# Optimization experiments

Hardware: AMD Instinct MI355X
Metric: run time of the kernel (lower is better)

Reference implementation:

```python
import jax, jax.numpy as jnp
import numpy as np

B, C, H, W = 8, 256, 64, 64
CR = C // 8  # reduced channels for query/key


def setup_inputs() -> dict:
    key = jax.random.key(0)
    ks = jax.random.split(key, 10)
    s = 0.02
    return {
        "x": jax.random.normal(ks[0], (B, C, H, W), dtype=jnp.float32),
        "cross_modal_features": jax.random.normal(ks[1], (B, C, H, W), dtype=jnp.float32),
        "wq": jax.random.normal(ks[2], (CR, C), dtype=jnp.float32) * s,
        "bq": jnp.zeros((CR,), dtype=jnp.float32),
        "wk": jax.random.normal(ks[3], (CR, C), dtype=jnp.float32) * s,
        "bk": jnp.zeros((CR,), dtype=jnp.float32),
        "wv": jax.random.normal(ks[4], (C, C), dtype=jnp.float32) * s,
        "bv": jnp.zeros((C,), dtype=jnp.float32),
        "wo": jax.random.normal(ks[5], (C, C), dtype=jnp.float32) * s,
        "bo": jnp.zeros((C,), dtype=jnp.float32),
        "gamma": jnp.zeros((1,), dtype=jnp.float32),
    }


def _conv1x1(w, b, t):
    # t: (B, Cin, HW) -> (B, Cout, HW); 1x1 conv == channel matmul
    return jnp.einsum("oc,bcn->bon", w, t) + b[None, :, None]


def reference(x, cross_modal_features, wq, bq, wk, bk, wv, bv, wo, bo, gamma):
    b, c, h, w = x.shape
    n = h * w
    xf = x.reshape(b, c, n)
    ff = cross_modal_features.reshape(b, c, n)
    q = _conv1x1(wq, bq, xf)          # (B, CR, N)
    k = _conv1x1(wk, bk, ff)          # (B, CR, N)
    v = _conv1x1(wv, bv, ff)          # (B, C, N)
    # attention[b,i,j] = softmax_j(q[b,:,i] . k[b,:,j])
    scores = jnp.einsum("bdi,bdj->bij", q, k)
    attn = jax.nn.softmax(scores, axis=-1)
    # out[b,c,i] = sum_j v[b,c,j] * attn[b,i,j]
    out = jnp.einsum("bcj,bij->bci", v, attn)
    out = _conv1x1(wo, bo, out).reshape(b, c, h, w)
    return gamma[0] * out + x
```

## Files before the change

kernel.cpp:

```cpp
#include <hip/hip_runtime.h>
#include <hip/hip_bf16.h>
#include <math.h>

#define B_  8
#define C_  256
#define CR_ 32
#define N_  4096

typedef __attribute__((ext_vector_type(8)))  short bf16x8;
typedef __attribute__((ext_vector_type(16))) float f32x16;
typedef __attribute__((ext_vector_type(4)))  int   int4v;

__device__ inline unsigned short f2b(float x) {
    __hip_bfloat16 h = __float2bfloat16(x);
    return __builtin_bit_cast(unsigned short, h);
}

#define GLL16(gsrc, ldst) \
    __builtin_amdgcn_global_load_lds((const __attribute__((address_space(1))) void*)(gsrc), \
                                     (__attribute__((address_space(3))) void*)(ldst), 16, 0, 0)

__global__ void pack_kernel(
    const float* __restrict__ wq, const float* __restrict__ bq,
    const float* __restrict__ wk, const float* __restrict__ bk,
    const float* __restrict__ wv, const float* __restrict__ bv,
    const float* __restrict__ wo,
    unsigned short* __restrict__ W1, unsigned short* __restrict__ W2,
    float* __restrict__ Bs1)
{
    const int r = blockIdx.x, t = threadIdx.x;
    const float L2E = 1.44269504088896340736f;
    if (r < 320) {
        float w;
        if (r < 32)      w = wq[r * C_ + t] * L2E;
        else if (r < 64) w = wk[(r - 32) * C_ + t];
        else             w = wv[(r - 64) * C_ + t];
        W1[r * C_ + t] = f2b(w);
        if (t == 0)
            Bs1[r] = (r < 32) ? bq[r] * L2E : ((r < 64) ? bk[r - 32] : bv[r - 64]);
    } else {
        W2[(r - 320) * C_ + t] = f2b(wo[(r - 320) * C_ + t]);
    }
}

__global__ __launch_bounds__(256) void convT_kernel(
    const float* __restrict__ x, const float* __restrict__ f,
    unsigned short* __restrict__ xT, unsigned short* __restrict__ fT)
{
    __shared__ float tile[64][65];
    const int t  = threadIdx.x;
    const int n0 = blockIdx.x * 64;
    const int c0 = blockIdx.y * 64;
    const int z  = blockIdx.z;
    const int b  = z >> 1;
    const float* src = (z & 1) ? f : x;
    unsigned short* dst = (z & 1) ? fT : xT;
    const size_t so = (size_t)b * C_ * N_;

    #pragma unroll
    for (int it = 0; it < 4; ++it) {
        const int cl = it * 16 + (t >> 4);
        *(float4*)&tile[cl][(t & 15) * 4] =
            *(const float4*)&src[so + (size_t)(c0 + cl) * N_ + n0 + (t & 15) * 4];
    }
    __syncthreads();

    const int nl = t >> 2;
    const int cg = (t & 3) * 16;
    unsigned short* drow = dst + ((size_t)b * N_ + n0 + nl) * C_ + c0 + cg;
    int4v w0, w1;
    #pragma unroll
    for (int e = 0; e < 4; ++e)
        w0[e] = (int)(((unsigned)f2b(tile[cg + 2*e][nl])) |
                      (((unsigned)f2b(tile[cg + 2*e + 1][nl])) << 16));
    #pragma unroll
    for (int e = 0; e < 4; ++e)
        w1[e] = (int)(((unsigned)f2b(tile[cg + 8 + 2*e][nl])) |
                      (((unsigned)f2b(tile[cg + 9 + 2*e][nl])) << 16));
    *(int4v*)(drow)     = w0;
    *(int4v*)(drow + 8) = w1;
}

__device__ __forceinline__ void gemm_mainloop(
    const unsigned short* __restrict__ Asrc,
    const unsigned short* __restrict__ Bsrc,
    unsigned short (*Ab)[32 * 32], unsigned short (*Bb)[256 * 32],
    int w, int l, f32x16& acc0, f32x16& acc1)
{
    const int jl = l & 31, hi = l >> 5;
    const int fj = (jl >> 1) & 3;

#define STAGE(KK, BUF) { \
    _Pragma("unroll") \
    for (int p = 0; p < 4; ++p) { \
        const int idx = p * 256 + w * 64 + l; \
        const int row = idx >> 2, slot = idx & 3; \
        GLL16(Bsrc + (size_t)row * 256 + (KK) * 32 + (slot ^ ((row >> 1) & 3)) * 8, \
              Bb[BUF] + (size_t)(p * 256 + w * 64) * 8); \
    } \
    if (w == 0) { \
        _Pragma("unroll") \
        for (int qq = 0; qq < 2; ++qq) { \
            const int idx = qq * 64 + l; \
            const int row = idx >> 2, slot = idx & 3; \
            GLL16(Asrc + (size_t)row * 256 + (KK) * 32 + (slot ^ ((row >> 1) & 3)) * 8, \
                  Ab[BUF] + (size_t)(qq * 64) * 8); \
        } \
    } }

    STAGE(0, 0)
    __syncthreads();

    for (int kk = 0; kk < 8; ++kk) {
        const int cur = kk & 1;
        if (kk < 7) STAGE(kk + 1, cur ^ 1)

        const unsigned short* Ac = Ab[cur];
        const unsigned short* Bc = Bb[cur];
        const bf16x8 af0 = *(const bf16x8*)&Ac[jl * 32 + ((hi ^ fj) * 8)];
        const bf16x8 af1 = *(const bf16x8*)&Ac[jl * 32 + (((2 + hi) ^ fj) * 8)];
        const int r0 = w * 64 + jl, r1 = w * 64 + 32 + jl;
        const bf16x8 bf00 = *(const bf16x8*)&Bc[r0 * 32 + ((hi ^ fj) * 8)];
        const bf16x8 bf01 = *(const bf16x8*)&Bc[r0 * 32 + (((2 + hi) ^ fj) * 8)];
        const bf16x8 bf10 = *(const bf16x8*)&Bc[r1 * 32 + ((hi ^ fj) * 8)];
        const bf16x8 bf11 = *(const bf16x8*)&Bc[r1 * 32 + (((2 + hi) ^ fj) * 8)];

        acc0 = __builtin_amdgcn_mfma_f32_32x32x16_bf16(af0, bf00, acc0, 0, 0, 0);
        acc0 = __builtin_amdgcn_mfma_f32_32x32x16_bf16(af1, bf01, acc0, 0, 0, 0);
        acc1 = __builtin_amdgcn_mfma_f32_32x32x16_bf16(af0, bf10, acc1, 0, 0, 0);
        acc1 = __builtin_amdgcn_mfma_f32_32x32x16_bf16(af1, bf11, acc1, 0, 0, 0);
        __syncthreads();
    }
#undef STAGE
}

__global__ __launch_bounds__(256) void qkv_gemm(
    const unsigned short* __restrict__ xT, const unsigned short* __restrict__ fT,
    const unsigned short* __restrict__ W1, const float* __restrict__ Bs1,
    unsigned short* __restrict__ qT, unsigned short* __restrict__ kT,
    unsigned short* __restrict__ v)
{
    __shared__ __align__(16) unsigned short Ab[2][32 * 32];
    __shared__ __align__(16) unsigned short Bb[2][256 * 32];

    const int t = threadIdx.x;
    const int w = t >> 6, l = t & 63;
    const int jl = l & 31, hi = l >> 5;
    const int bid = blockIdx.x;
    const int b  = bid & 7;
    const int r_ = bid >> 3;
    const int mt = r_ % 10;
    const int nt = r_ / 10;

    const unsigned short* Asrc = W1 + (size_t)mt * 32 * C_;
    const unsigned short* Bsrc = ((mt == 0) ? xT : fT) + (size_t)b * N_ * C_
                               + (size_t)nt * 256 * C_;

    f32x16 acc0 = (f32x16)0.f, acc1 = (f32x16)0.f;
    gemm_mainloop(Asrc, Bsrc, Ab, Bb, w, l, acc0, acc1);

    const int m0 = mt * 32;
    const int nb = nt * 256 + w * 64;
    if (mt <= 1) {
        unsigned short* dst = ((mt == 0) ? qT : kT) + (size_t)b * N_ * CR_;
        #pragma unroll
        for (int ns = 0; ns < 2; ++ns) {
            const f32x16& A = ns ? acc1 : acc0;
            const int n = nb + ns * 32 + jl;
            #pragma unroll
            for (int r4 = 0; r4 < 4; ++r4) {
                const float4 bi = *(const float4*)&Bs1[m0 + r4 * 8 + 4 * hi];
                const unsigned int d0 = (unsigned)f2b(A[r4*4+0] + bi.x) |
                                        ((unsigned)f2b(A[r4*4+1] + bi.y) << 16);
                const unsigned int d1 = (unsigned)f2b(A[r4*4+2] + bi.z) |
                                        ((unsigned)f2b(A[r4*4+3] + bi.w) << 16);
                *(uint2*)(dst + (size_t)n * CR_ + r4 * 8 + 4 * hi) = make_uint2(d0, d1);
            }
        }
    } else {
        unsigned short* dst = v + (size_t)b * C_ * N_;
        #pragma unroll
        for (int ns = 0; ns < 2; ++ns) {
            const f32x16& A = ns ? acc1 : acc0;
            const int n = nb + ns * 32 + jl;
            #pragma unroll
            for (int r4 = 0; r4 < 4; ++r4) {
                const float4 bi = *(const float4*)&Bs1[m0 + r4 * 8 + 4 * hi];
                #pragma unroll
                for (int e = 0; e < 4; ++e) {
                    const int c = m0 - 64 + e + 8 * r4 + 4 * hi;
                    dst[(size_t)c * N_ + n] = f2b(A[r4*4+e] + ((const float*)&bi)[e]);
                }
            }
        }
    }
}

__device__ inline void softmax_tile(const f32x16& s, float& lsum,
                                    bf16x8& pf0, bf16x8& pf1)
{
    float ps = 0.f;
    int wd[8];
    #pragma unroll
    for (int r = 0; r < 16; r += 2) {
        float e0 = __builtin_amdgcn_exp2f(s[r]);
        float e1 = __builtin_amdgcn_exp2f(s[r + 1]);
        ps += e0 + e1;
        int pk;
        asm("v_cvt_pk_bf16_f32 %0, %1, %2" : "=v"(pk) : "v"(e0), "v"(e1));
        wd[r >> 1] = pk;
    }
    lsum += ps;
    asm volatile("v_permlane32_swap_b32 %0, %1" : "+v"(wd[0]), "+v"(wd[2]));
    asm volatile("v_permlane32_swap_b32 %0, %1" : "+v"(wd[1]), "+v"(wd[3]));
    asm volatile("v_permlane32_swap_b32 %0, %1" : "+v"(wd[4]), "+v"(wd[6]));
    asm volatile("v_permlane32_swap_b32 %0, %1" : "+v"(wd[5]), "+v"(wd[7]));
    union { int4v i4; bf16x8 h8; } u0, u1;
    u0.i4 = (int4v){ wd[0], wd[1], wd[2], wd[3] };
    u1.i4 = (int4v){ wd[4], wd[5], wd[6], wd[7] };
    pf0 = u0.h8; pf1 = u1.h8;
}

__global__ __launch_bounds__(512) void attn_kernel(
    const unsigned short* __restrict__ qT, const unsigned short* __restrict__ kT,
    const unsigned short* __restrict__ v, unsigned short* __restrict__ aoT)
{
    __shared__ __align__(16) unsigned short Vt[2][256 * 64];
    __shared__ __align__(16) unsigned short Kt[2][64 * 32];

    const int t  = threadIdx.x;
    const int w  = t >> 6;
    const int l  = t & 63;
    const int jl = l & 31;
    const int hi = l >> 5;
    const int ig = w >> 1;
    const int cs = w & 1;

    const int bid = blockIdx.x;
    const int b   = bid & 7;
    const int it  = bid >> 3;
    const int i   = it * 128 + ig * 32 + jl;

    const unsigned short* qTb = qT + (size_t)b * N_ * CR_;
    const unsigned short* kTb = kT + (size_t)b * N_ * CR_;
    const unsigned short* vb  = v  + (size_t)b * C_ * N_;

    const bf16x8 qa0 = *(const bf16x8*)(qTb + (size_t)i * CR_ + hi * 8);
    const bf16x8 qa1 = *(const bf16x8*)(qTb + (size_t)i * CR_ + 16 + hi * 8);

    const unsigned short* vsrc[4];
    int vdst[4];
    #pragma unroll
    for (int p = 0; p < 4; ++p) {
        const int idx = p * 512 + w * 64 + l;
        const int row = idx >> 3, slot = idx & 7;
        vsrc[p] = vb + (size_t)row * N_ + (slot ^ (row & 7)) * 8;
        vdst[p] = idx * 8;
    }
    const int kidx = w * 64 + l;
    const int krow = kidx >> 2, kslot = kidx & 3;
    const unsigned short* ksrc = kTb + (size_t)krow * CR_ + (kslot ^ ((krow >> 1) & 3)) * 8;

    f32x16 acc0 = (f32x16)0.f, acc1 = (f32x16)0.f;
    f32x16 acc2 = (f32x16)0.f, acc3 = (f32x16)0.f;
    float lsa = 0.f;

    #pragma unroll
    for (int p = 0; p < 4; ++p) GLL16(vsrc[p], &Vt[0][vdst[p]]);
    if (w < 4) GLL16(ksrc, &Kt[0][kidx * 8]);
    __syncthreads();

    const int fj = (jl >> 1) & 3;
    int vrow[4];
    #pragma unroll
    for (int ct = 0; ct < 4; ++ct) vrow[ct] = cs * 128 + ct * 32 + jl;

    for (int jt = 0; jt < N_ / 64; ++jt) {
        const int cur = jt & 1;
        if (jt + 1 < N_ / 64) {
            const int nxt = cur ^ 1;
            const size_t jn = (size_t)(jt + 1) * 64;
            #pragma unroll
            for (int p = 0; p < 4; ++p) GLL16(vsrc[p] + jn, &Vt[nxt][vdst[p]]);
            if (w < 4) GLL16(ksrc + jn * CR_, &Kt[nxt][kidx * 8]);
        }

        #pragma unroll
        for (int h = 0; h < 2; ++h) {
            const int kbase = (h * 32 + jl) * 32;
            const bf16x8 kf0 = *(const bf16x8*)&Kt[cur][kbase + ((hi ^ fj) * 8)];
            const bf16x8 kf1 = *(const bf16x8*)&Kt[cur][kbase + (((2 + hi) ^ fj) * 8)];
            __builtin_amdgcn_s_setprio(1);
            f32x16 sa = (f32x16)0.f;
            sa = __builtin_amdgcn_mfma_f32_32x32x16_bf16(kf0, qa0, sa, 0, 0, 0);
            sa = __builtin_amdgcn_mfma_f32_32x32x16_bf16(kf1, qa1, sa, 0, 0, 0);
            __builtin_amdgcn_s_setprio(0);

            bf16x8 pa0, pa1;
            softmax_tile(sa, lsa, pa0, pa1);

            __builtin_amdgcn_s_setprio(1);
            #pragma unroll
            for (int ct = 0; ct < 4; ++ct) {
                const int r = vrow[ct];
                const bf16x8 v0 = *(const bf16x8*)
                    &Vt[cur][r * 64 + (((4 * h + hi) ^ (r & 7)) * 8)];
                const bf16x8 v1 = *(const bf16x8*)
                    &Vt[cur][r * 64 + (((4 * h + 2 + hi) ^ (r & 7)) * 8)];
                f32x16& A = (ct == 0) ? acc0 : (ct == 1) ? acc1 : (ct == 2) ? acc2 : acc3;
                A = __builtin_amdgcn_mfma_f32_32x32x16_bf16(v0, pa0, A, 0, 0, 0);
                A = __builtin_amdgcn_mfma_f32_32x32x16_bf16(v1, pa1, A, 0, 0, 0);
            }
            __builtin_amdgcn_s_setprio(0);
        }

        __syncthreads();
    }

    lsa += __shfl_xor(lsa, 32);
    const float ra = 1.f / lsa;
    unsigned short* aoTb = aoT + (size_t)b * N_ * C_;
#define EPI(ACC, CT) { _Pragma("unroll") \
    for (int r4 = 0; r4 < 4; ++r4) { \
        const unsigned int d0 = (unsigned)f2b(ACC[r4*4+0] * ra) | \
                                ((unsigned)f2b(ACC[r4*4+1] * ra) << 16); \
        const unsigned int d1 = (unsigned)f2b(ACC[r4*4+2] * ra) | \
                                ((unsigned)f2b(ACC[r4*4+3] * ra) << 16); \
        *(uint2*)(aoTb + (size_t)i * C_ + cs * 128 + (CT) * 32 + r4 * 8 + 4 * hi) \
            = make_uint2(d0, d1); } }
    EPI(acc0, 0)
    EPI(acc1, 1)
    EPI(acc2, 2)
    EPI(acc3, 3)
#undef EPI
}

__global__ __launch_bounds__(256) void out_gemm(
    const unsigned short* __restrict__ aoT, const unsigned short* __restrict__ W2,
    const float* __restrict__ bo, const float* __restrict__ gamma,
    const float* __restrict__ x, float* __restrict__ out)
{
    __shared__ __align__(16) unsigned short Ab[2][32 * 32];
    __shared__ __align__(16) unsigned short Bb[2][256 * 32];

    const int t = threadIdx.x;
    const int w = t >> 6, l = t & 63;
    const int jl = l & 31, hi = l >> 5;
    const int bid = blockIdx.x;
    const int b  = bid & 7;
    const int r_ = bid >> 3;
    const int mt = r_ & 7;
    const int nt = r_ >> 3;

    const unsigned short* Asrc = W2 + (size_t)mt * 32 * C_;
    const unsigned short* Bsrc = aoT + (size_t)b * N_ * C_ + (size_t)nt * 256 * C_;

    f32x16 acc0 = (f32x16)0.f, acc1 = (f32x16)0.f;
    gemm_mainloop(Asrc, Bsrc, Ab, Bb, w, l, acc0, acc1);

    const float gm = gamma[0];
    const int m0 = mt * 32;
    const int nb = nt * 256 + w * 64;
    #pragma unroll
    for (int ns = 0; ns < 2; ++ns) {
        const f32x16& A = ns ? acc1 : acc0;
        const int n = nb + ns * 32 + jl;
        #pragma unroll
        for (int r4 = 0; r4 < 4; ++r4) {
            const float4 bi = *(const float4*)&bo[m0 + r4 * 8 + 4 * hi];
            #pragma unroll
            for (int e = 0; e < 4; ++e) {
                const int c = m0 + e + 8 * r4 + 4 * hi;
                const size_t o = ((size_t)b * C_ + c) * N_ + n;
                out[o] = fmaf(gm, A[r4*4+e] + ((const float*)&bi)[e], x[o]);
            }
        }
    }
}

extern "C" void kernel_launch(void* const* d_in, const int* in_sizes, int n_in,
                              void* d_out, int out_size, void* d_ws, size_t ws_size,
                              hipStream_t stream)
{
    const float* x     = (const float*)d_in[0];
    const float* f     = (const float*)d_in[1];
    const float* wq    = (const float*)d_in[2];
    const float* bq    = (const float*)d_in[3];
    const float* wk    = (const float*)d_in[4];
    const float* bk    = (const float*)d_in[5];
    const float* wv    = (const float*)d_in[6];
    const float* bv    = (const float*)d_in[7];
    const float* wo    = (const float*)d_in[8];
    const float* bo    = (const float*)d_in[9];
    const float* gamma = (const float*)d_in[10];
    float* out = (float*)d_out;

    float* Bs1 = (float*)d_ws;
    unsigned short* W1 = (unsigned short*)(Bs1 + 320);
    unsigned short* W2 = W1 + 320 * C_;
    unsigned short* xT = W2 + 256 * C_;
    unsigned short* fT = xT + (size_t)B_ * N_ * C_;
    unsigned short* qT = fT + (size_t)B_ * N_ * C_;
    unsigned short* kT = qT + (size_t)B_ * N_ * CR_;
    unsigned short* vv = kT + (size_t)B_ * N_ * CR_;
    unsigned short* aoT = vv + (size_t)B_ * C_ * N_;

    pack_kernel<<<dim3(576), 256, 0, stream>>>(wq, bq, wk, bk, wv, bv, wo, W1, W2, Bs1);
    convT_kernel<<<dim3(64, 4, 16), 256, 0, stream>>>(x, f, xT, fT);
    qkv_gemm<<<dim3(1280), 256, 0, stream>>>(xT, fT, W1, Bs1, qT, kT, vv);
    attn_kernel<<<dim3(256), 512, 0, stream>>>(qT, kT, vv, aoT);
    out_gemm<<<dim3(1024), 256, 0, stream>>>(aoT, W2, bo, gamma, x, out);
}
```

Before: 169.4 us.

## Load K fragments directly into registers and batch both score tiles per step

Drops the shared-memory staging of K. Each lane now loads its K fragments straight from global memory into registers, with a register double buffer that prefetches the next tile. The two 32-column score halves are computed together before softmax, then all the PV MFMAs run in one loop. This removes the LDS traffic and swizzle for K and gives more independent MFMA work between the two phases, at the cost of extra registers and redundant global K loads across waves.

```diff
diff --git a/kernel.cpp b/kernel.cpp
--- a/kernel.cpp
+++ b/kernel.cpp
@@ -226,7 +226,6 @@
     const unsigned short* __restrict__ v, unsigned short* __restrict__ aoT)
 {
     __shared__ __align__(16) unsigned short Vt[2][256 * 64];
-    __shared__ __align__(16) unsigned short Kt[2][64 * 32];
 
     const int t  = threadIdx.x;
     const int w  = t >> 6;
@@ -248,6 +247,8 @@
     const bf16x8 qa0 = *(const bf16x8*)(qTb + (size_t)i * CR_ + hi * 8);
     const bf16x8 qa1 = *(const bf16x8*)(qTb + (size_t)i * CR_ + 16 + hi * 8);
 
+    const unsigned short* kln = kTb + (size_t)jl * CR_ + hi * 8;
+
     const unsigned short* vsrc[4];
     int vdst[4];
     #pragma unroll
@@ -257,9 +258,6 @@
         vsrc[p] = vb + (size_t)row * N_ + (slot ^ (row & 7)) * 8;
         vdst[p] = idx * 8;
     }
-    const int kidx = w * 64 + l;
-    const int krow = kidx >> 2, kslot = kidx & 3;
-    const unsigned short* ksrc = kTb + (size_t)krow * CR_ + (kslot ^ ((krow >> 1) & 3)) * 8;
 
     f32x16 acc0 = (f32x16)0.f, acc1 = (f32x16)0.f;
     f32x16 acc2 = (f32x16)0.f, acc3 = (f32x16)0.f;
@@ -267,54 +265,65 @@
 
     #pragma unroll
     for (int p = 0; p < 4; ++p) GLL16(vsrc[p], &Vt[0][vdst[p]]);
-    if (w < 4) GLL16(ksrc, &Kt[0][kidx * 8]);
+    bf16x8 kc00 = *(const bf16x8*)(kln);
+    bf16x8 kc01 = *(const bf16x8*)(kln + 16);
+    bf16x8 kc10 = *(const bf16x8*)(kln + 32 * CR_);
+    bf16x8 kc11 = *(const bf16x8*)(kln + 32 * CR_ + 16);
     __syncthreads();
 
-    const int fj = (jl >> 1) & 3;
     int vrow[4];
     #pragma unroll
     for (int ct = 0; ct < 4; ++ct) vrow[ct] = cs * 128 + ct * 32 + jl;
 
     for (int jt = 0; jt < N_ / 64; ++jt) {
         const int cur = jt & 1;
+        bf16x8 kn00 = kc00, kn01 = kc01, kn10 = kc10, kn11 = kc11;
         if (jt + 1 < N_ / 64) {
             const int nxt = cur ^ 1;
             const size_t jn = (size_t)(jt + 1) * 64;
             #pragma unroll
             for (int p = 0; p < 4; ++p) GLL16(vsrc[p] + jn, &Vt[nxt][vdst[p]]);
-            if (w < 4) GLL16(ksrc + jn * CR_, &Kt[nxt][kidx * 8]);
+            const unsigned short* kp = kln + jn * CR_;
+            kn00 = *(const bf16x8*)(kp);
+            kn01 = *(const bf16x8*)(kp + 16);
+            kn10 = *(const bf16x8*)(kp + 32 * CR_);
+            kn11 = *(const bf16x8*)(kp + 32 * CR_ + 16);
         }
 
+        __builtin_amdgcn_s_setprio(1);
+        f32x16 s0 = (f32x16)0.f, s1 = (f32x16)0.f;
+        s0 = __builtin_amdgcn_mfma_f32_32x32x16_bf16(kc00, qa0, s0, 0, 0, 0);
+        s0 = __builtin_amdgcn_mfma_f32_32x32x16_bf16(kc01, qa1, s0, 0, 0, 0);
+        s1 = __builtin_amdgcn_mfma_f32_32x32x16_bf16(kc10, qa0, s1, 0, 0, 0);
+        s1 = __builtin_amdgcn_mfma_f32_32x32x16_bf16(kc11, qa1, s1, 0, 0, 0);
+        __builtin_amdgcn_s_setprio(0);
+
+        bf16x8 p00, p01, p10, p11;
+        softmax_tile(s0, lsa, p00, p01);
+        softmax_tile(s1, lsa, p10, p11);
+
+        __builtin_amdgcn_s_setprio(1);
         #pragma unroll
-        for (int h = 0; h < 2; ++h) {
-            const int kbase = (h * 32 + jl) * 32;
-            const bf16x8 kf0 = *(const bf16x8*)&Kt[cur][kbase + ((hi ^ fj) * 8)];
-            const bf16x8 kf1 = *(const bf16x8*)&Kt[cur][kbase + (((2 + hi) ^ fj) * 8)];
-            __builtin_amdgcn_s_setprio(1);
-            f32x16 sa = (f32x16)0.f;
-            sa = __builtin_amdgcn_mfma_f32_32x32x16_bf16(kf0, qa0, sa, 0, 0, 0);
-            sa = __builtin_amdgcn_mfma_f32_32x32x16_bf16(kf1, qa1, sa, 0, 0, 0);
-            __builtin_amdgcn_s_setprio(0);
-
-            bf16x8 pa0, pa1;
-            softmax_tile(sa, lsa, pa0, pa1);
-
-            __builtin_amdgcn_s_setprio(1);
-            #pragma unroll
-            for (int ct = 0; ct < 4; ++ct) {
-                const int r = vrow[ct];
-                const bf16x8 v0 = *(const bf16x8*)
-                    &Vt[cur][r * 64 + (((4 * h + hi) ^ (r & 7)) * 8)];
-                const bf16x8 v1 = *(const bf16x8*)
-                    &Vt[cur][r * 64 + (((4 * h + 2 + hi) ^ (r & 7)) * 8)];
-                f32x16& A = (ct == 0) ? acc0 : (ct == 1) ? acc1 : (ct == 2) ? acc2 : acc3;
-                A = __builtin_amdgcn_mfma_f32_32x32x16_bf16(v0, pa0, A, 0, 0, 0);
-                A = __builtin_amdgcn_mfma_f32_32x32x16_bf16(v1, pa1, A, 0, 0, 0);
-            }
-            __builtin_amdgcn_s_setprio(0);
+        for (int ct = 0; ct < 4; ++ct) {
+            const int r = vrow[ct];
+            const bf16x8 v00 = *(const bf16x8*)
+                &Vt[cur][r * 64 + ((hi ^ (r & 7)) * 8)];
+            const bf16x8 v01 = *(const bf16x8*)
+                &Vt[cur][r * 64 + (((2 + hi) ^ (r & 7)) * 8)];
+            const bf16x8 v10 = *(const bf16x8*)
+                &Vt[cur][r * 64 + (((4 + hi) ^ (r & 7)) * 8)];
+            const bf16x8 v11 = *(const bf16x8*)
+                &Vt[cur][r * 64 + (((6 + hi) ^ (r & 7)) * 8)];
+            f32x16& A = (ct == 0) ? acc0 : (ct == 1) ? acc1 : (ct == 2) ? acc2 : acc3;
+            A = __builtin_amdgcn_mfma_f32_32x32x16_bf16(v00, p00, A, 0, 0, 0);
+            A = __builtin_amdgcn_mfma_f32_32x32x16_bf16(v01, p01, A, 0, 0, 0);
+            A = __builtin_amdgcn_mfma_f32_32x32x16_bf16(v10, p10, A, 0, 0, 0);
+            A = __builtin_amdgcn_mfma_f32_32x32x16_bf16(v11, p11, A, 0, 0, 0);
         }
+        __builtin_amdgcn_s_setprio(0);
 
         __syncthreads();
+        kc00 = kn00; kc01 = kn01; kc10 = kn10; kc11 = kn11;
     }
 
     lsa += __shfl_xor(lsa, 32);
```

New measurement: 161.4 us. 1.05x faster.

## Load K fragments directly to registers and double the V tile to 128 keys

Applied to the files above, without the earlier changes.

K is no longer staged through shared memory. Each lane now loads its K fragment straight from global memory into registers, and the next sub-tile's fragment is prefetched one step ahead. The V tile per iteration grows from 64 to 128 keys, which halves the number of loop iterations and block-wide barriers. Shared memory use rises to 128 KB of double-buffered V, which may limit occupancy, and K loads now come from global or L2 inside the inner loop.

```diff
diff --git a/kernel.cpp b/kernel.cpp
--- a/kernel.cpp
+++ b/kernel.cpp
@@ -225,8 +225,7 @@
     const unsigned short* __restrict__ qT, const unsigned short* __restrict__ kT,
     const unsigned short* __restrict__ v, unsigned short* __restrict__ aoT)
 {
-    __shared__ __align__(16) unsigned short Vt[2][256 * 64];
-    __shared__ __align__(16) unsigned short Kt[2][64 * 32];
+    __shared__ __align__(16) unsigned short Vt[2][256 * 128];
 
     const int t  = threadIdx.x;
     const int w  = t >> 6;
@@ -248,70 +247,72 @@
     const bf16x8 qa0 = *(const bf16x8*)(qTb + (size_t)i * CR_ + hi * 8);
     const bf16x8 qa1 = *(const bf16x8*)(qTb + (size_t)i * CR_ + 16 + hi * 8);
 
-    const unsigned short* vsrc[4];
-    int vdst[4];
-    #pragma unroll
-    for (int p = 0; p < 4; ++p) {
-        const int idx = p * 512 + w * 64 + l;
-        const int row = idx >> 3, slot = idx & 7;
+    const unsigned short* kln = kTb + (size_t)jl * CR_ + hi * 8;
+
+    const unsigned short* vsrc[8];
+    int vdst[8];
+    #pragma unroll
+    for (int p = 0; p < 8; ++p) {
+        const int idx = p * 512 + t;
+        const int row = idx >> 4, slot = idx & 15;
         vsrc[p] = vb + (size_t)row * N_ + (slot ^ (row & 7)) * 8;
         vdst[p] = idx * 8;
     }
-    const int kidx = w * 64 + l;
-    const int krow = kidx >> 2, kslot = kidx & 3;
-    const unsigned short* ksrc = kTb + (size_t)krow * CR_ + (kslot ^ ((krow >> 1) & 3)) * 8;
 
     f32x16 acc0 = (f32x16)0.f, acc1 = (f32x16)0.f;
     f32x16 acc2 = (f32x16)0.f, acc3 = (f32x16)0.f;
     float lsa = 0.f;
 
     #pragma unroll
-    for (int p = 0; p < 4; ++p) GLL16(vsrc[p], &Vt[0][vdst[p]]);
-    if (w < 4) GLL16(ksrc, &Kt[0][kidx * 8]);
+    for (int p = 0; p < 8; ++p) GLL16(vsrc[p], &Vt[0][vdst[p]]);
+    bf16x8 kc0 = *(const bf16x8*)(kln);
+    bf16x8 kc1 = *(const bf16x8*)(kln + 16);
     __syncthreads();
 
-    const int fj = (jl >> 1) & 3;
     int vrow[4];
     #pragma unroll
     for (int ct = 0; ct < 4; ++ct) vrow[ct] = cs * 128 + ct * 32 + jl;
 
-    for (int jt = 0; jt < N_ / 64; ++jt) {
+    for (int jt = 0; jt < N_ / 128; ++jt) {
         const int cur = jt & 1;
-        if (jt + 1 < N_ / 64) {
-            const int nxt = cur ^ 1;
-            const size_t jn = (size_t)(jt + 1) * 64;
+        if (jt + 1 < N_ / 128) {
+            const size_t jn = (size_t)(jt + 1) * 128;
             #pragma unroll
-            for (int p = 0; p < 4; ++p) GLL16(vsrc[p] + jn, &Vt[nxt][vdst[p]]);
-            if (w < 4) GLL16(ksrc + jn * CR_, &Kt[nxt][kidx * 8]);
+            for (int p = 0; p < 8; ++p) GLL16(vsrc[p] + jn, &Vt[cur ^ 1][vdst[p]]);
         }
 
         #pragma unroll
-        for (int h = 0; h < 2; ++h) {
-            const int kbase = (h * 32 + jl) * 32;
-            const bf16x8 kf0 = *(const bf16x8*)&Kt[cur][kbase + ((hi ^ fj) * 8)];
-            const bf16x8 kf1 = *(const bf16x8*)&Kt[cur][kbase + (((2 + hi) ^ fj) * 8)];
+        for (int sub = 0; sub < 4; ++sub) {
+            const size_t koff = (sub < 3)
+                ? ((size_t)jt * 128 + (sub + 1) * 32) * CR_
+                : ((jt + 1 < N_ / 128) ? (size_t)(jt + 1) * 128 * CR_ : 0);
+            const bf16x8 kn0 = *(const bf16x8*)(kln + koff);
+            const bf16x8 kn1 = *(const bf16x8*)(kln + koff + 16);
+
             __builtin_amdgcn_s_setprio(1);
-            f32x16 sa = (f32x16)0.f;
-            sa = __builtin_amdgcn_mfma_f32_32x32x16_bf16(kf0, qa0, sa, 0, 0, 0);
-            sa = __builtin_amdgcn_mfma_f32_32x32x16_bf16(kf1, qa1, sa, 0, 0, 0);
+            f32x16 s = (f32x16)0.f;
+            s = __builtin_amdgcn_mfma_f32_32x32x16_bf16(kc0, qa0, s, 0, 0, 0);
+            s = __builtin_amdgcn_mfma_f32_32x32x16_bf16(kc1, qa1, s, 0, 0, 0);
             __builtin_amdgcn_s_setprio(0);
 
-            bf16x8 pa0, pa1;
-            softmax_tile(sa, lsa, pa0, pa1);
+            bf16x8 p0, p1;
+            softmax_tile(s, lsa, p0, p1);
 
             __builtin_amdgcn_s_setprio(1);
             #pragma unroll
             for (int ct = 0; ct < 4; ++ct) {
                 const int r = vrow[ct];
                 const bf16x8 v0 = *(const bf16x8*)
-                    &Vt[cur][r * 64 + (((4 * h + hi) ^ (r & 7)) * 8)];
+                    &Vt[cur][r * 128 + (((sub * 4 + hi) ^ (r & 7)) * 8)];
                 const bf16x8 v1 = *(const bf16x8*)
-                    &Vt[cur][r * 64 + (((4 * h + 2 + hi) ^ (r & 7)) * 8)];
+                    &Vt[cur][r * 128 + (((sub * 4 + 2 + hi) ^ (r & 7)) * 8)];
                 f32x16& A = (ct == 0) ? acc0 : (ct == 1) ? acc1 : (ct == 2) ? acc2 : acc3;
-                A = __builtin_amdgcn_mfma_f32_32x32x16_bf16(v0, pa0, A, 0, 0, 0);
-                A = __builtin_amdgcn_mfma_f32_32x32x16_bf16(v1, pa1, A, 0, 0, 0);
+                A = __builtin_amdgcn_mfma_f32_32x32x16_bf16(v0, p0, A, 0, 0, 0);
+                A = __builtin_amdgcn_mfma_f32_32x32x16_bf16(v1, p1, A, 0, 0, 0);
             }
             __builtin_amdgcn_s_setprio(0);
+
+            kc0 = kn0; kc1 = kn1;
         }
 
         __syncthreads();
```

New measurement: 170.0 us. About the same (+0.4%).

## Split key range across wave pairs and reuse V fragments over two query tiles

Applied to the files above, without the earlier changes.

Each wave now handles 64 query rows and half of each 64-key tile, so every V fragment read from LDS feeds two query tiles instead of one. K fragments are loaded straight from global into registers with a one-tile prefetch, replacing the K shared-memory staging. Partial accumulators and row sums from the two key halves are combined through LDS at the end. This doubles the accumulator registers per wave and adds an LDS reduction with extra barriers, which may reduce occupancy.

```diff
diff --git a/kernel.cpp b/kernel.cpp
--- a/kernel.cpp
+++ b/kernel.cpp
@@ -226,113 +226,150 @@
     const unsigned short* __restrict__ v, unsigned short* __restrict__ aoT)
 {
     __shared__ __align__(16) unsigned short Vt[2][256 * 64];
-    __shared__ __align__(16) unsigned short Kt[2][64 * 32];
+    __shared__ float lsx[2][512];
 
     const int t  = threadIdx.x;
     const int w  = t >> 6;
     const int l  = t & 63;
     const int jl = l & 31;
     const int hi = l >> 5;
-    const int ig = w >> 1;
-    const int cs = w & 1;
+    const int js = w & 1;
+    const int ig = (w >> 1) & 1;
+    const int cs = w >> 2;
 
     const int bid = blockIdx.x;
     const int b   = bid & 7;
     const int it  = bid >> 3;
-    const int i   = it * 128 + ig * 32 + jl;
+    const int i0  = it * 128 + ig * 64;
 
     const unsigned short* qTb = qT + (size_t)b * N_ * CR_;
     const unsigned short* kTb = kT + (size_t)b * N_ * CR_;
     const unsigned short* vb  = v  + (size_t)b * C_ * N_;
 
-    const bf16x8 qa0 = *(const bf16x8*)(qTb + (size_t)i * CR_ + hi * 8);
-    const bf16x8 qa1 = *(const bf16x8*)(qTb + (size_t)i * CR_ + 16 + hi * 8);
+    const bf16x8 q00 = *(const bf16x8*)(qTb + (size_t)(i0 + jl) * CR_ + hi * 8);
+    const bf16x8 q01 = *(const bf16x8*)(qTb + (size_t)(i0 + jl) * CR_ + 16 + hi * 8);
+    const bf16x8 q10 = *(const bf16x8*)(qTb + (size_t)(i0 + 32 + jl) * CR_ + hi * 8);
+    const bf16x8 q11 = *(const bf16x8*)(qTb + (size_t)(i0 + 32 + jl) * CR_ + 16 + hi * 8);
+
+    const unsigned short* kln = kTb + (size_t)(js * 32 + jl) * CR_ + hi * 8;
 
     const unsigned short* vsrc[4];
     int vdst[4];
     #pragma unroll
     for (int p = 0; p < 4; ++p) {
-        const int idx = p * 512 + w * 64 + l;
+        const int idx = p * 512 + t;
         const int row = idx >> 3, slot = idx & 7;
         vsrc[p] = vb + (size_t)row * N_ + (slot ^ (row & 7)) * 8;
         vdst[p] = idx * 8;
     }
-    const int kidx = w * 64 + l;
-    const int krow = kidx >> 2, kslot = kidx & 3;
-    const unsigned short* ksrc = kTb + (size_t)krow * CR_ + (kslot ^ ((krow >> 1) & 3)) * 8;
-
-    f32x16 acc0 = (f32x16)0.f, acc1 = (f32x16)0.f;
-    f32x16 acc2 = (f32x16)0.f, acc3 = (f32x16)0.f;
-    float lsa = 0.f;
+
+    f32x16 a00 = (f32x16)0.f, a01 = (f32x16)0.f, a02 = (f32x16)0.f, a03 = (f32x16)0.f;
+    f32x16 a10 = (f32x16)0.f, a11 = (f32x16)0.f, a12 = (f32x16)0.f, a13 = (f32x16)0.f;
+    float ls0 = 0.f, ls1 = 0.f;
 
     #pragma unroll
     for (int p = 0; p < 4; ++p) GLL16(vsrc[p], &Vt[0][vdst[p]]);
-    if (w < 4) GLL16(ksrc, &Kt[0][kidx * 8]);
-    __syncthreads();
-
-    const int fj = (jl >> 1) & 3;
-    int vrow[4];
-    #pragma unroll
-    for (int ct = 0; ct < 4; ++ct) vrow[ct] = cs * 128 + ct * 32 + jl;
+    bf16x8 kc0 = *(const bf16x8*)(kln);
+    bf16x8 kc1 = *(const bf16x8*)(kln + 16);
+    __syncthreads();
+
+    int voff0[4], voff1[4];
+    #pragma unroll
+    for (int ct = 0; ct < 4; ++ct) {
+        const int rv = cs * 128 + ct * 32 + jl;
+        voff0[ct] = rv * 64 + (((js * 4 + hi)     ^ (rv & 7)) * 8);
+        voff1[ct] = rv * 64 + (((js * 4 + 2 + hi) ^ (rv & 7)) * 8);
+    }
 
     for (int jt = 0; jt < N_ / 64; ++jt) {
         const int cur = jt & 1;
+        bf16x8 kn0 = kc0, kn1 = kc1;
         if (jt + 1 < N_ / 64) {
-            const int nxt = cur ^ 1;
             const size_t jn = (size_t)(jt + 1) * 64;
             #pragma unroll
-            for (int p = 0; p < 4; ++p) GLL16(vsrc[p] + jn, &Vt[nxt][vdst[p]]);
-            if (w < 4) GLL16(ksrc + jn * CR_, &Kt[nxt][kidx * 8]);
+            for (int p = 0; p < 4; ++p) GLL16(vsrc[p] + jn, &Vt[cur ^ 1][vdst[p]]);
+            kn0 = *(const bf16x8*)(kln + jn * CR_);
+            kn1 = *(const bf16x8*)(kln + jn * CR_ + 16);
         }
 
-        #pragma unroll
-        for (int h = 0; h < 2; ++h) {
-            const int kbase = (h * 32 + jl) * 32;
-            const bf16x8 kf0 = *(const bf16x8*)&Kt[cur][kbase + ((hi ^ fj) * 8)];
-            const bf16x8 kf1 = *(const bf16x8*)&Kt[cur][kbase + (((2 + hi) ^ fj) * 8)];
-            __builtin_amdgcn_s_setprio(1);
-            f32x16 sa = (f32x16)0.f;
-            sa = __builtin_amdgcn_mfma_f32_32x32x16_bf16(kf0, qa0, sa, 0, 0, 0);
-            sa = __builtin_amdgcn_mfma_f32_32x32x16_bf16(kf1, qa1, sa, 0, 0, 0);
-            __builtin_amdgcn_s_setprio(0);
-
-            bf16x8 pa0, pa1;
-            softmax_tile(sa, lsa, pa0, pa1);
-
-            __builtin_amdgcn_s_setprio(1);
-            #pragma unroll
-            for (int ct = 0; ct < 4; ++ct) {
-                const int r = vrow[ct];
-                const bf16x8 v0 = *(const bf16x8*)
-                    &Vt[cur][r * 64 + (((4 * h + hi) ^ (r & 7)) * 8)];
-                const bf16x8 v1 = *(const bf16x8*)
-                    &Vt[cur][r * 64 + (((4 * h + 2 + hi) ^ (r & 7)) * 8)];
-                f32x16& A = (ct == 0) ? acc0 : (ct == 1) ? acc1 : (ct == 2) ? acc2 : acc3;
-                A = __builtin_amdgcn_mfma_f32_32x32x16_bf16(v0, pa0, A, 0, 0, 0);
-                A = __builtin_amdgcn_mfma_f32_32x32x16_bf16(v1, pa1, A, 0, 0, 0);
-            }
-            __builtin_amdgcn_s_setprio(0);
-        }
+        __builtin_amdgcn_s_setprio(1);
+        f32x16 s0 = (f32x16)0.f, s1 = (f32x16)0.f;
+        s0 = __builtin_amdgcn_mfma_f32_32x32x16_bf16(kc0, q00, s0, 0, 0, 0);
+        s0 = __builtin_amdgcn_mfma_f32_32x32x16_bf16(kc1, q01, s0, 0, 0, 0);
+        s1 = __builtin_amdgcn_mfma_f32_32x32x16_bf16(kc0, q10, s1, 0, 0, 0);
+        s1 = __builtin_amdgcn_mfma_f32_32x32x16_bf16(kc1, q11, s1, 0, 0, 0);
+        __builtin_amdgcn_s_setprio(0);
+
+        bf16x8 p00, p01, p10, p11;
+        softmax_tile(s0, ls0, p00, p01);
+        softmax_tile(s1, ls1, p10, p11);
+
+        __builtin_amdgcn_s_setprio(1);
+#define PVSTEP(CT, AA, AB) { \
+        const bf16x8 v0_ = *(const bf16x8*)&Vt[cur][voff0[CT]]; \
+        const bf16x8 v1_ = *(const bf16x8*)&Vt[cur][voff1[CT]]; \
+        AA = __builtin_amdgcn_mfma_f32_32x32x16_bf16(v0_, p00, AA, 0, 0, 0); \
+        AA = __builtin_amdgcn_mfma_f32_32x32x16_bf16(v1_, p01, AA, 0, 0, 0); \
+        AB = __builtin_amdgcn_mfma_f32_32x32x16_bf16(v0_, p10, AB, 0, 0, 0); \
+        AB = __builtin_amdgcn_mfma_f32_32x32x16_bf16(v1_, p11, AB, 0, 0, 0); }
+        PVSTEP(0, a00, a10)
+        PVSTEP(1, a01, a11)
+        PVSTEP(2, a02, a12)
+        PVSTEP(3, a03, a13)
+#undef PVSTEP
+        __builtin_amdgcn_s_setprio(0);
 
         __syncthreads();
-    }
-
-    lsa += __shfl_xor(lsa, 32);
-    const float ra = 1.f / lsa;
-    unsigned short* aoTb = aoT + (size_t)b * N_ * C_;
-#define EPI(ACC, CT) { _Pragma("unroll") \
+        kc0 = kn0; kc1 = kn1;
+    }
+
+    ls0 += __shfl_xor(ls0, 32);
+    ls1 += __shfl_xor(ls1, 32);
+
+    lsx[0][w * 64 + l] = ls0;
+    lsx[1][w * 64 + l] = ls1;
+    float* As = (float*)&Vt[0][0];
+    const int base = (w >> 1) * 4096;
+
+#define STORE_ACC(A, CT) { _Pragma("unroll") \
+    for (int r = 0; r < 16; ++r) As[base + (CT) * 1024 + r * 64 + l] = A[r]; }
+#define ADD_ACC(A, CT) { _Pragma("unroll") \
+    for (int r = 0; r < 16; ++r) A[r] += As[base + (CT) * 1024 + r * 64 + l]; }
+
+    __syncthreads();
+    if (js == 1) { STORE_ACC(a00, 0) STORE_ACC(a01, 1) STORE_ACC(a02, 2) STORE_ACC(a03, 3) }
+    __syncthreads();
+    if (js == 0) { ADD_ACC(a00, 0) ADD_ACC(a01, 1) ADD_ACC(a02, 2) ADD_ACC(a03, 3) }
+    __syncthreads();
+    if (js == 1) { STORE_ACC(a10, 0) STORE_ACC(a11, 1) STORE_ACC(a12, 2) STORE_ACC(a13, 3) }
+    __syncthreads();
+    if (js == 0) {
+        ADD_ACC(a10, 0) ADD_ACC(a11, 1) ADD_ACC(a12, 2) ADD_ACC(a13, 3)
+
+        const float ra = 1.f / (ls0 + lsx[0][(w + 1) * 64 + l]);
+        const float rb = 1.f / (ls1 + lsx[1][(w + 1) * 64 + l]);
+        unsigned short* aoTb = aoT + (size_t)b * N_ * C_;
+        const int ica = i0 + jl, icb = i0 + 32 + jl;
+#define EPI(ACC, CT, COL, RL) { _Pragma("unroll") \
     for (int r4 = 0; r4 < 4; ++r4) { \
-        const unsigned int d0 = (unsigned)f2b(ACC[r4*4+0] * ra) | \
-                                ((unsigned)f2b(ACC[r4*4+1] * ra) << 16); \
-        const unsigned int d1 = (unsigned)f2b(ACC[r4*4+2] * ra) | \
-                                ((unsigned)f2b(ACC[r4*4+3] * ra) << 16); \
-        *(uint2*)(aoTb + (size_t)i * C_ + cs * 128 + (CT) * 32 + r4 * 8 + 4 * hi) \
+        const unsigned int d0 = (unsigned)f2b(ACC[r4*4+0] * (RL)) | \
+                                ((unsigned)f2b(ACC[r4*4+1] * (RL)) << 16); \
+        const unsigned int d1 = (unsigned)f2b(ACC[r4*4+2] * (RL)) | \
+                                ((unsigned)f2b(ACC[r4*4+3] * (RL)) << 16); \
+        *(uint2*)(aoTb + (size_t)(COL) * C_ + cs * 128 + (CT) * 32 + r4 * 8 + 4 * hi) \
             = make_uint2(d0, d1); } }
-    EPI(acc0, 0)
-    EPI(acc1, 1)
-    EPI(acc2, 2)
-    EPI(acc3, 3)
+        EPI(a00, 0, ica, ra)
+        EPI(a01, 1, ica, ra)
+        EPI(a02, 2, ica, ra)
+        EPI(a03, 3, ica, ra)
+        EPI(a10, 0, icb, rb)
+        EPI(a11, 1, icb, rb)
+        EPI(a12, 2, icb, rb)
+        EPI(a13, 3, icb, rb)
 #undef EPI
+    }
+#undef STORE_ACC
+#undef ADD_ACC
 }
 
 __global__ __launch_bounds__(256) void out_gemm(
```

Result: faster. 159.6 us (-5.8%).
